# Kernel tuning notes

Hardware: AMD Instinct MI355X
Metric: run time of the kernel (lower is better)

## Reference

```python
import jax, jax.numpy as jnp
import numpy as np

N = 100_000
E = 3_200_000
NCLASS = 64
TOPK = 16
NHID = 128
DEGREE = 6


def setup_inputs() -> dict:
    key = jax.random.key(0)
    ks = jax.random.split(key, 8)
    x = jax.random.normal(ks[0], (N, NCLASS), dtype=jnp.float32)
    edge_row = jax.random.randint(ks[1], (E,), 0, N, dtype=jnp.int64)
    edge_col = jax.random.randint(ks[2], (E,), 0, N, dtype=jnp.int64)
    edge_val = jax.random.uniform(ks[3], (E,), dtype=jnp.float32) / 32.0  # ~row-normalized
    # torch.nn.Linear init: U(-1/sqrt(fan_in), 1/sqrt(fan_in))
    lim1 = 1.0 / np.sqrt(TOPK)
    lim2 = 1.0 / np.sqrt(NHID)
    W1 = jax.random.uniform(ks[4], (NHID, TOPK), jnp.float32, -lim1, lim1)
    b1 = jnp.zeros((NHID,), jnp.float32)
    W2 = jax.random.uniform(ks[5], (DEGREE, NHID), jnp.float32, -lim2, lim2)
    b2 = jnp.zeros((DEGREE,), jnp.float32)
    return {"x": x, "edge_row": edge_row, "edge_col": edge_col,
            "edge_val": edge_val, "W1": W1, "b1": b1, "W2": W2, "b2": b2}


def _spmm(edge_row, edge_col, edge_val, h):
    # (adj @ h)[i] = sum_{(i,j) in E} val_ij * h[j]
    return jax.ops.segment_sum(edge_val[:, None] * h[edge_col], edge_row,
                               num_segments=N)


def reference(x, edge_row, edge_col, edge_val, W1, b1, W2, b2):
    # gating: softmax over classes -> top-k probs -> small MLP -> hop weights
    p = jax.nn.softmax(x, axis=1)
    tk, _ = jax.lax.top_k(p, TOPK)                       # [N, TOPK]
    h = jax.nn.leaky_relu(tk @ W1.T + b1, 0.1)           # [N, NHID]
    weight = jax.nn.softmax(h @ W2.T + b2, axis=1)       # [N, DEGREE]
    # dropout is identity in eval mode
    out = weight[:, 0:1] * x
    cur = x
    for i in range(DEGREE - 1):
        cur = _spmm(edge_row, edge_col, edge_val, cur)
        out = out + weight[:, i + 1:i + 2] * cur
    return jax.nn.log_softmax(out, axis=1)
```

## Files before the change

kernel.cpp:

```cpp
#include <hip/hip_runtime.h>
#include <math.h>

#define N_NODES 100000
#define N_EDGES 3200000
#define NCLASS  64
#define TOPK    16
#define NHID    128
#define DEG     6

#define NBUCK   391
#define BUCKCAP 9216

__device__ __forceinline__ float bf2f(unsigned short u) {
    return __uint_as_float(((unsigned)u) << 16);
}
__device__ __forceinline__ unsigned short f2bf(float f) {
    unsigned u = __float_as_uint(f);
    u = (u + 0x7FFFu + ((u >> 16) & 1u)) >> 16;
    return (unsigned short)u;
}

__device__ __forceinline__ float wave_max(float v) {
    #pragma unroll
    for (int off = 1; off < 64; off <<= 1) v = fmaxf(v, __shfl_xor(v, off));
    return v;
}
__device__ __forceinline__ float wave_sum(float v) {
    #pragma unroll
    for (int off = 1; off < 64; off <<= 1) v += __shfl_xor(v, off);
    return v;
}

__global__ void phase1_bucket(const int* __restrict__ erow, const int* __restrict__ ecol,
                              const float* __restrict__ eval, int* __restrict__ fill,
                              int2* __restrict__ staging) {
    int i = blockIdx.x * 256 + threadIdx.x;
    if (i < N_EDGES) {
        int   r = __builtin_nontemporal_load(&erow[i]);
        int   c = __builtin_nontemporal_load(&ecol[i]);
        float w = __builtin_nontemporal_load(&eval[i]);
        int b = r >> 8;
        int pos = atomicAdd(&fill[b * 16], 1);
        if (pos < BUCKCAP) {
            int2 e;
            e.x = (c << 8) | (r & 255);
            e.y = __float_as_int(w);
            staging[(size_t)b * BUCKCAP + pos] = e;
        }
    }
}

__global__ void bucket_scan(const int* __restrict__ fill, int* __restrict__ bucket_base,
                            int* __restrict__ row_ptr) {
    __shared__ int sdat[512];
    int tid = threadIdx.x;
    int c = 0;
    if (tid < NBUCK) c = min(fill[tid * 16], BUCKCAP);
    sdat[tid] = c;
    __syncthreads();
    for (int off = 1; off < 512; off <<= 1) {
        int t = (tid >= off) ? sdat[tid - off] : 0;
        __syncthreads();
        sdat[tid] += t;
        __syncthreads();
    }
    if (tid < NBUCK) bucket_base[tid] = sdat[tid] - c;
    if (tid == 0) row_ptr[N_NODES] = sdat[511];
}

__global__ __launch_bounds__(256) void phase2_build(
        const int2* __restrict__ staging, const int* __restrict__ fill,
        const int* __restrict__ bucket_base, int* __restrict__ row_ptr,
        int2* __restrict__ edges_s) {
    __shared__ int lhist[256];
    __shared__ int lscan[256];
    __shared__ int lfill[256];
    int b = blockIdx.x, tid = threadIdx.x;
    int c = min(fill[b * 16], BUCKCAP);
    const int2* seg = staging + (size_t)b * BUCKCAP;
    lhist[tid] = 0;
    __syncthreads();
    for (int j = tid; j < c; j += 256) atomicAdd(&lhist[seg[j].x & 255], 1);
    __syncthreads();
    int v = lhist[tid];
    lscan[tid] = v;
    __syncthreads();
    for (int off = 1; off < 256; off <<= 1) {
        int t = (tid >= off) ? lscan[tid - off] : 0;
        __syncthreads();
        lscan[tid] += t;
        __syncthreads();
    }
    int excl = bucket_base[b] + (lscan[tid] - v);
    int grow = b * 256 + tid;
    if (grow < N_NODES) row_ptr[grow] = excl;
    lfill[tid] = excl;
    __syncthreads();
    for (int j = tid; j < c; j += 256) {
        int2 e = seg[j];
        int rl = e.x & 255;
        int pos = atomicAdd(&lfill[rl], 1);
        edges_s[pos] = make_int2((int)(((unsigned)e.x) >> 8), e.y);
    }
}

#define GNODES 32
__global__ __launch_bounds__(256) void gating_kernel(
        const float* __restrict__ x,  const float* __restrict__ W1,
        const float* __restrict__ b1, const float* __restrict__ W2,
        const float* __restrict__ b2, float* __restrict__ weight,
        float* __restrict__ out_acc, unsigned short* __restrict__ xbf) {
    __shared__ float sW1t[TOPK * NHID];
    __shared__ float sb1[NHID];
    __shared__ float sW2[DEG * NHID];
    __shared__ float sb2[DEG];
    int tid = threadIdx.x;
    for (int idx = tid; idx < NHID * TOPK; idx += 256) {
        int k = idx / NHID, j = idx - k * NHID;
        sW1t[idx] = W1[j * TOPK + k];
    }
    for (int i = tid; i < NHID; i += 256) sb1[i] = b1[i];
    for (int i = tid; i < DEG * NHID; i += 256) sW2[i] = W2[i];
    if (tid < DEG) sb2[tid] = b2[tid];
    __syncthreads();

    int wave = tid >> 6;
    int lane = tid & 63;

    for (int it = 0; it < GNODES / 4; it++) {
        int node = blockIdx.x * GNODES + it * 4 + wave;
        if (node >= N_NODES) continue;

        float xv = x[node * NCLASS + lane];
        xbf[node * NCLASS + lane] = f2bf(xv);

        float v = xv;
        #pragma unroll
        for (int k = 2; k <= 64; k <<= 1) {
            #pragma unroll
            for (int j = k >> 1; j > 0; j >>= 1) {
                float o = __shfl_xor(v, j);
                bool keep_small = (((lane & j) == 0) == ((lane & k) == 0));
                v = keep_small ? fminf(v, o) : fmaxf(v, o);
            }
        }
        float m = __shfl(v, 63);
        float e = __expf(v - m);
        float s = wave_sum(e);
        float inv_s = 1.0f / s;

        float h0 = sb1[lane], h1 = sb1[lane + 64];
        #pragma unroll
        for (int k = 0; k < TOPK; k++) {
            float sv = __shfl(v, 63 - k);
            float tk = __expf(sv - m) * inv_s;
            h0 += tk * sW1t[k * NHID + lane];
            h1 += tk * sW1t[k * NHID + lane + 64];
        }
        h0 = (h0 > 0.f) ? h0 : 0.1f * h0;
        h1 = (h1 > 0.f) ? h1 : 0.1f * h1;

        float w[DEG];
        float wm = -1e30f;
        #pragma unroll
        for (int d = 0; d < DEG; d++) {
            float part = h0 * sW2[d * NHID + lane] + h1 * sW2[d * NHID + lane + 64];
            w[d] = wave_sum(part) + sb2[d];
            wm = fmaxf(wm, w[d]);
        }
        float wsum = 0.f;
        #pragma unroll
        for (int d = 0; d < DEG; d++) { w[d] = __expf(w[d] - wm); wsum += w[d]; }
        float inv = 1.0f / wsum;

        if (lane < DEG) weight[node * DEG + lane] = w[lane] * inv;
        out_acc[node * NCLASS + lane] = w[0] * inv * xv;
    }
}

__device__ __forceinline__ void gather8(const unsigned short* __restrict__ src,
                                        const long long* __restrict__ edq,
                                        int e, int lane, float& acc) {
    long long q[8];
    #pragma unroll
    for (int k = 0; k < 8; k++) q[k] = __builtin_nontemporal_load(&edq[e + k]);
    float vk[8], fk[8];
    #pragma unroll
    for (int k = 0; k < 8; k++) {
        int col = __builtin_amdgcn_readfirstlane((int)(unsigned)q[k]);
        vk[k] = __int_as_float(__builtin_amdgcn_readfirstlane((int)(q[k] >> 32)));
        fk[k] = bf2f(src[col * NCLASS + lane]);
    }
    #pragma unroll
    for (int k = 0; k < 8; k++) acc += vk[k] * fk[k];
}

__device__ __forceinline__ void gather4(const unsigned short* __restrict__ src,
                                        const long long* __restrict__ edq,
                                        int e, int lane, float& acc) {
    long long q[4];
    #pragma unroll
    for (int k = 0; k < 4; k++) q[k] = __builtin_nontemporal_load(&edq[e + k]);
    float vk[4], fk[4];
    #pragma unroll
    for (int k = 0; k < 4; k++) {
        int col = __builtin_amdgcn_readfirstlane((int)(unsigned)q[k]);
        vk[k] = __int_as_float(__builtin_amdgcn_readfirstlane((int)(q[k] >> 32)));
        fk[k] = bf2f(src[col * NCLASS + lane]);
    }
    #pragma unroll
    for (int k = 0; k < 4; k++) acc += vk[k] * fk[k];
}

__device__ __forceinline__ float drain_row(const unsigned short* __restrict__ src,
                                           const long long* __restrict__ edq,
                                           int e, int end, int lane, float acc) {
    for (; e + 4 <= end; e += 4) gather4(src, edq, e, lane, acc);
    for (; e < end; e++) {
        long long q0 = __builtin_nontemporal_load(&edq[e]);
        int   c0 = __builtin_amdgcn_readfirstlane((int)(unsigned)q0);
        float v0 = __int_as_float(__builtin_amdgcn_readfirstlane((int)(q0 >> 32)));
        acc += v0 * bf2f(src[c0 * NCLASS + lane]);
    }
    return acc;
}

__global__ __launch_bounds__(256) void spmm_kernel(
        const unsigned short* __restrict__ src, unsigned short* __restrict__ dst,
        const int* __restrict__ row_ptr, const int2* __restrict__ edges_s,
        const float* __restrict__ weight,
        float* __restrict__ out_acc, float* __restrict__ final_out,
        int hop, int mode) {
    int wave = threadIdx.x >> 6;
    int lane = threadIdx.x & 63;
    int wid = blockIdx.x * 4 + wave;
    int rA = wid * 2;
    if (rA >= N_NODES) return;
    int rB = rA + 1;

    int sA   = __builtin_amdgcn_readfirstlane(row_ptr[rA]);
    int endA = __builtin_amdgcn_readfirstlane(row_ptr[rA + 1]);
    int endB = __builtin_amdgcn_readfirstlane(row_ptr[rA + 2]);

    const long long* edq = (const long long*)edges_s;
    float accA = 0.f, accB = 0.f;
    int eA = sA, eB = endA;
    while (eA + 8 <= endA && eB + 8 <= endB) {
        gather8(src, edq, eA, lane, accA);
        gather8(src, edq, eB, lane, accB);
        eA += 8; eB += 8;
    }
    accA = drain_row(src, edq, eA, endA, lane, accA);
    accB = drain_row(src, edq, eB, endB, lane, accB);

    float wA = weight[rA * DEG + hop];
    float wB = weight[rB * DEG + hop];
    if (mode == 0) {
        dst[rA * NCLASS + lane] = f2bf(accA);
        dst[rB * NCLASS + lane] = f2bf(accB);
    } else if (mode == 1) {
        dst[rA * NCLASS + lane] = f2bf(accA);
        dst[rB * NCLASS + lane] = f2bf(accB);
        float pA = bf2f(src[rA * NCLASS + lane]);
        float pB = bf2f(src[rB * NCLASS + lane]);
        float wpA = weight[rA * DEG + hop - 1];
        float wpB = weight[rB * DEG + hop - 1];
        out_acc[rA * NCLASS + lane] += wpA * pA + wA * accA;
        out_acc[rB * NCLASS + lane] += wpB * pB + wB * accB;
    } else {
        float vA = out_acc[rA * NCLASS + lane] + wA * accA;
        float mA = wave_max(vA);
        float eA2 = __expf(vA - mA);
        float sA2 = wave_sum(eA2);
        final_out[rA * NCLASS + lane] = vA - mA - __logf(sA2);

        float vB = out_acc[rB * NCLASS + lane] + wB * accB;
        float mB = wave_max(vB);
        float eB2 = __expf(vB - mB);
        float sB2 = wave_sum(eB2);
        final_out[rB * NCLASS + lane] = vB - mB - __logf(sB2);
    }
}

extern "C" void kernel_launch(void* const* d_in, const int* in_sizes, int n_in,
                              void* d_out, int out_size, void* d_ws, size_t ws_size,
                              hipStream_t stream) {
    const float* x    = (const float*)d_in[0];
    const int*   erow = (const int*)  d_in[1];
    const int*   ecol = (const int*)  d_in[2];
    const float* eval = (const float*)d_in[3];
    const float* W1   = (const float*)d_in[4];
    const float* b1   = (const float*)d_in[5];
    const float* W2   = (const float*)d_in[6];
    const float* b2   = (const float*)d_in[7];
    float* out = (float*)d_out;

    char* ws = (char*)d_ws;
    size_t off = 0;
    auto alloc = [&](size_t bytes) -> void* {
        void* p = ws + off;
        off = (off + bytes + 255) & ~(size_t)255;
        return p;
    };
    char* regionA = (char*)alloc((size_t)N_NODES * NCLASS * 2 * 3);
    int2* staging = (int2*)regionA;
    unsigned short* xbf  = (unsigned short*)regionA;
    unsigned short* cur0 = (unsigned short*)(regionA + (size_t)N_NODES * NCLASS * 2);
    unsigned short* cur1 = (unsigned short*)(regionA + (size_t)N_NODES * NCLASS * 4);

    int2*  edges_s     = (int2*)alloc((size_t)N_EDGES * 8);
    int*   row_ptr     = (int*) alloc((size_t)(N_NODES + 1) * 4);
    int*   fill        = (int*) alloc((size_t)NBUCK * 16 * 4);
    int*   bucket_base = (int*) alloc((size_t)NBUCK * 4);
    float* weight      = (float*)alloc((size_t)N_NODES * DEG * 4);

    const int EB = (N_EDGES + 255) / 256;
    const int WB = ((N_NODES / 2) + 3) / 4;
    const int GB = (N_NODES + GNODES - 1) / GNODES;

    hipMemsetAsync(fill, 0, (size_t)NBUCK * 16 * 4, stream);
    phase1_bucket<<<EB, 256, 0, stream>>>(erow, ecol, eval, fill, staging);
    bucket_scan<<<1, 512, 0, stream>>>(fill, bucket_base, row_ptr);
    phase2_build<<<NBUCK, 256, 0, stream>>>(staging, fill, bucket_base, row_ptr, edges_s);

    gating_kernel<<<GB, 256, 0, stream>>>(x, W1, b1, W2, b2, weight, out, xbf);

    spmm_kernel<<<WB, 256, 0, stream>>>(xbf,  cur0, row_ptr, edges_s, weight, out, out, 1, 0);
    spmm_kernel<<<WB, 256, 0, stream>>>(cur0, cur1, row_ptr, edges_s, weight, out, out, 2, 1);
    spmm_kernel<<<WB, 256, 0, stream>>>(cur1, cur0, row_ptr, edges_s, weight, out, out, 3, 0);
    spmm_kernel<<<WB, 256, 0, stream>>>(cur0, cur1, row_ptr, edges_s, weight, out, out, 4, 1);
    spmm_kernel<<<WB, 256, 0, stream>>>(cur1, cur0, row_ptr, edges_s, weight, out, out, 5, 2);
}
```

Baseline: 722.1 us.

## Fuse edge bucketing with gating, split bucket atomics, fold accumulation into final hop

Merges the edge-bucketing pass and the gating MLP into one launch by partitioning the grid. Bucket fill counters are split into 8 sub-segments so fewer edges contend on each atomic. The separate scan kernel is dropped, and each build block instead computes its own base by summing the counts of earlier buckets. Hop 4 no longer does its out_acc read-modify-write; the final hop reads the two previous hop outputs and applies their weights, which saves a full pass over the fp32 accumulator. The costs are redundant prefix work in every build block and larger staging capacity limits, since edges beyond a sub-segment's capacity are silently dropped.

```diff
diff --git a/kernel.cpp b/kernel.cpp
--- a/kernel.cpp
+++ b/kernel.cpp
@@ -9,7 +9,12 @@
 #define DEG     6
 
 #define NBUCK   391
-#define BUCKCAP 9216
+#define NSEG    8
+#define SEGCAP  1408
+
+#define EB ((N_EDGES + 255) / 256)
+#define GNODES 32
+#define GB ((N_NODES + GNODES - 1) / GNODES)
 
 __device__ __forceinline__ float bf2f(unsigned short u) {
     return __uint_as_float(((unsigned)u) << 16);
@@ -31,81 +36,10 @@
     return v;
 }
 
-__global__ void phase1_bucket(const int* __restrict__ erow, const int* __restrict__ ecol,
-                              const float* __restrict__ eval, int* __restrict__ fill,
-                              int2* __restrict__ staging) {
-    int i = blockIdx.x * 256 + threadIdx.x;
-    if (i < N_EDGES) {
-        int   r = __builtin_nontemporal_load(&erow[i]);
-        int   c = __builtin_nontemporal_load(&ecol[i]);
-        float w = __builtin_nontemporal_load(&eval[i]);
-        int b = r >> 8;
-        int pos = atomicAdd(&fill[b * 16], 1);
-        if (pos < BUCKCAP) {
-            int2 e;
-            e.x = (c << 8) | (r & 255);
-            e.y = __float_as_int(w);
-            staging[(size_t)b * BUCKCAP + pos] = e;
-        }
-    }
-}
-
-__global__ void bucket_scan(const int* __restrict__ fill, int* __restrict__ bucket_base,
-                            int* __restrict__ row_ptr) {
-    __shared__ int sdat[512];
-    int tid = threadIdx.x;
-    int c = 0;
-    if (tid < NBUCK) c = min(fill[tid * 16], BUCKCAP);
-    sdat[tid] = c;
-    __syncthreads();
-    for (int off = 1; off < 512; off <<= 1) {
-        int t = (tid >= off) ? sdat[tid - off] : 0;
-        __syncthreads();
-        sdat[tid] += t;
-        __syncthreads();
-    }
-    if (tid < NBUCK) bucket_base[tid] = sdat[tid] - c;
-    if (tid == 0) row_ptr[N_NODES] = sdat[511];
-}
-
-__global__ __launch_bounds__(256) void phase2_build(
-        const int2* __restrict__ staging, const int* __restrict__ fill,
-        const int* __restrict__ bucket_base, int* __restrict__ row_ptr,
-        int2* __restrict__ edges_s) {
-    __shared__ int lhist[256];
-    __shared__ int lscan[256];
-    __shared__ int lfill[256];
-    int b = blockIdx.x, tid = threadIdx.x;
-    int c = min(fill[b * 16], BUCKCAP);
-    const int2* seg = staging + (size_t)b * BUCKCAP;
-    lhist[tid] = 0;
-    __syncthreads();
-    for (int j = tid; j < c; j += 256) atomicAdd(&lhist[seg[j].x & 255], 1);
-    __syncthreads();
-    int v = lhist[tid];
-    lscan[tid] = v;
-    __syncthreads();
-    for (int off = 1; off < 256; off <<= 1) {
-        int t = (tid >= off) ? lscan[tid - off] : 0;
-        __syncthreads();
-        lscan[tid] += t;
-        __syncthreads();
-    }
-    int excl = bucket_base[b] + (lscan[tid] - v);
-    int grow = b * 256 + tid;
-    if (grow < N_NODES) row_ptr[grow] = excl;
-    lfill[tid] = excl;
-    __syncthreads();
-    for (int j = tid; j < c; j += 256) {
-        int2 e = seg[j];
-        int rl = e.x & 255;
-        int pos = atomicAdd(&lfill[rl], 1);
-        edges_s[pos] = make_int2((int)(((unsigned)e.x) >> 8), e.y);
-    }
-}
-
-#define GNODES 32
-__global__ __launch_bounds__(256) void gating_kernel(
+__global__ __launch_bounds__(256) void scatter_gating_kernel(
+        const int* __restrict__ erow, const int* __restrict__ ecol,
+        const float* __restrict__ eval, int* __restrict__ fill,
+        int2* __restrict__ staging,
         const float* __restrict__ x,  const float* __restrict__ W1,
         const float* __restrict__ b1, const float* __restrict__ W2,
         const float* __restrict__ b2, float* __restrict__ weight,
@@ -114,6 +48,26 @@
     __shared__ float sb1[NHID];
     __shared__ float sW2[DEG * NHID];
     __shared__ float sb2[DEG];
+
+    if (blockIdx.x < EB) {
+        int i = blockIdx.x * 256 + threadIdx.x;
+        int s = blockIdx.x & 7;
+        if (i < N_EDGES) {
+            int   r = __builtin_nontemporal_load(&erow[i]);
+            int   c = __builtin_nontemporal_load(&ecol[i]);
+            float w = __builtin_nontemporal_load(&eval[i]);
+            int b = r >> 8;
+            int pos = atomicAdd(&fill[(s * NBUCK + b) * 16], 1);
+            if (pos < SEGCAP) {
+                int2 e;
+                e.x = (c << 8) | (r & 255);
+                e.y = __float_as_int(w);
+                staging[((size_t)b * NSEG + s) * SEGCAP + pos] = e;
+            }
+        }
+        return;
+    }
+
     int tid = threadIdx.x;
     for (int idx = tid; idx < NHID * TOPK; idx += 256) {
         int k = idx / NHID, j = idx - k * NHID;
@@ -126,9 +80,10 @@
 
     int wave = tid >> 6;
     int lane = tid & 63;
+    int gb = blockIdx.x - EB;
 
     for (int it = 0; it < GNODES / 4; it++) {
-        int node = blockIdx.x * GNODES + it * 4 + wave;
+        int node = gb * GNODES + it * 4 + wave;
         if (node >= N_NODES) continue;
 
         float xv = x[node * NCLASS + lane];
@@ -175,6 +130,67 @@
 
         if (lane < DEG) weight[node * DEG + lane] = w[lane] * inv;
         out_acc[node * NCLASS + lane] = w[0] * inv * xv;
+    }
+}
+
+__global__ __launch_bounds__(256) void phase2_build(
+        const int2* __restrict__ staging, const int* __restrict__ fill,
+        int* __restrict__ row_ptr, int2* __restrict__ edges_s) {
+    __shared__ int lred[256];
+    __shared__ int lhist[256];
+    __shared__ int lscan[256];
+    __shared__ int lfill[256];
+    __shared__ int sseg[NSEG];
+    int b = blockIdx.x, tid = threadIdx.x;
+
+    int part = 0;
+    for (int j = tid; j < b; j += 256) {
+        int t = 0;
+        #pragma unroll
+        for (int s = 0; s < NSEG; s++) t += min(fill[(s * NBUCK + j) * 16], SEGCAP);
+        part += t;
+    }
+    lred[tid] = part;
+    if (tid < NSEG) sseg[tid] = min(fill[(tid * NBUCK + b) * 16], SEGCAP);
+    __syncthreads();
+    for (int off = 128; off > 0; off >>= 1) {
+        if (tid < off) lred[tid] += lred[tid + off];
+        __syncthreads();
+    }
+    int base_b = lred[0];
+
+    lhist[tid] = 0;
+    __syncthreads();
+    for (int s = 0; s < NSEG; s++) {
+        int c = sseg[s];
+        const int2* seg = staging + ((size_t)b * NSEG + s) * SEGCAP;
+        for (int j = tid; j < c; j += 256) atomicAdd(&lhist[seg[j].x & 255], 1);
+    }
+    __syncthreads();
+    int v = lhist[tid];
+    lscan[tid] = v;
+    __syncthreads();
+    for (int off = 1; off < 256; off <<= 1) {
+        int t = (tid >= off) ? lscan[tid - off] : 0;
+        __syncthreads();
+        lscan[tid] += t;
+        __syncthreads();
+    }
+    int excl = base_b + (lscan[tid] - v);
+    int grow = b * 256 + tid;
+    if (grow < N_NODES) row_ptr[grow] = excl;
+    if (b == NBUCK - 1 && tid == 255) row_ptr[N_NODES] = excl + v;
+    lfill[tid] = excl;
+    __syncthreads();
+    for (int s = 0; s < NSEG; s++) {
+        int c = sseg[s];
+        const int2* seg = staging + ((size_t)b * NSEG + s) * SEGCAP;
+        for (int j = tid; j < c; j += 256) {
+            int2 e = seg[j];
+            int rl = e.x & 255;
+            int pos = atomicAdd(&lfill[rl], 1);
+            edges_s[pos] = make_int2((int)(((unsigned)e.x) >> 8), e.y);
+        }
     }
 }
 
@@ -227,6 +243,7 @@
 
 __global__ __launch_bounds__(256) void spmm_kernel(
         const unsigned short* __restrict__ src, unsigned short* __restrict__ dst,
+        const unsigned short* __restrict__ prev2,
         const int* __restrict__ row_ptr, const int2* __restrict__ edges_s,
         const float* __restrict__ weight,
         float* __restrict__ out_acc, float* __restrict__ final_out,
@@ -268,13 +285,21 @@
         out_acc[rA * NCLASS + lane] += wpA * pA + wA * accA;
         out_acc[rB * NCLASS + lane] += wpB * pB + wB * accB;
     } else {
-        float vA = out_acc[rA * NCLASS + lane] + wA * accA;
+        float p1A = bf2f(src[rA * NCLASS + lane]);
+        float p1B = bf2f(src[rB * NCLASS + lane]);
+        float p2A = bf2f(prev2[rA * NCLASS + lane]);
+        float p2B = bf2f(prev2[rB * NCLASS + lane]);
+        float vA = out_acc[rA * NCLASS + lane]
+                 + weight[rA * DEG + hop - 2] * p2A
+                 + weight[rA * DEG + hop - 1] * p1A + wA * accA;
         float mA = wave_max(vA);
         float eA2 = __expf(vA - mA);
         float sA2 = wave_sum(eA2);
         final_out[rA * NCLASS + lane] = vA - mA - __logf(sA2);
 
-        float vB = out_acc[rB * NCLASS + lane] + wB * accB;
+        float vB = out_acc[rB * NCLASS + lane]
+                 + weight[rB * DEG + hop - 2] * p2B
+                 + weight[rB * DEG + hop - 1] * p1B + wB * accB;
         float mB = wave_max(vB);
         float eB2 = __expf(vB - mB);
         float sB2 = wave_sum(eB2);
@@ -302,32 +327,27 @@
         off = (off + bytes + 255) & ~(size_t)255;
         return p;
     };
-    char* regionA = (char*)alloc((size_t)N_NODES * NCLASS * 2 * 3);
-    int2* staging = (int2*)regionA;
-    unsigned short* xbf  = (unsigned short*)regionA;
-    unsigned short* cur0 = (unsigned short*)(regionA + (size_t)N_NODES * NCLASS * 2);
-    unsigned short* cur1 = (unsigned short*)(regionA + (size_t)N_NODES * NCLASS * 4);
-
-    int2*  edges_s     = (int2*)alloc((size_t)N_EDGES * 8);
-    int*   row_ptr     = (int*) alloc((size_t)(N_NODES + 1) * 4);
-    int*   fill        = (int*) alloc((size_t)NBUCK * 16 * 4);
-    int*   bucket_base = (int*) alloc((size_t)NBUCK * 4);
-    float* weight      = (float*)alloc((size_t)N_NODES * DEG * 4);
-
-    const int EB = (N_EDGES + 255) / 256;
+    char* regionS = (char*)alloc((size_t)NBUCK * NSEG * SEGCAP * 8);
+    int2* staging = (int2*)regionS;
+    unsigned short* cur0 = (unsigned short*)regionS;
+    unsigned short* cur1 = (unsigned short*)(regionS + (size_t)N_NODES * NCLASS * 2);
+    unsigned short* xbf  = (unsigned short*)alloc((size_t)N_NODES * NCLASS * 2);
+
+    int2*  edges_s = (int2*)alloc((size_t)N_EDGES * 8);
+    int*   row_ptr = (int*) alloc((size_t)(N_NODES + 1) * 4);
+    int*   fill    = (int*) alloc((size_t)NSEG * NBUCK * 16 * 4);
+    float* weight  = (float*)alloc((size_t)N_NODES * DEG * 4);
+
     const int WB = ((N_NODES / 2) + 3) / 4;
-    const int GB = (N_NODES + GNODES - 1) / GNODES;
-
-    hipMemsetAsync(fill, 0, (size_t)NBUCK * 16 * 4, stream);
-    phase1_bucket<<<EB, 256, 0, stream>>>(erow, ecol, eval, fill, staging);
-    bucket_scan<<<1, 512, 0, stream>>>(fill, bucket_base, row_ptr);
-    phase2_build<<<NBUCK, 256, 0, stream>>>(staging, fill, bucket_base, row_ptr, edges_s);
-
-    gating_kernel<<<GB, 256, 0, stream>>>(x, W1, b1, W2, b2, weight, out, xbf);
-
-    spmm_kernel<<<WB, 256, 0, stream>>>(xbf,  cur0, row_ptr, edges_s, weight, out, out, 1, 0);
-    spmm_kernel<<<WB, 256, 0, stream>>>(cur0, cur1, row_ptr, edges_s, weight, out, out, 2, 1);
-    spmm_kernel<<<WB, 256, 0, stream>>>(cur1, cur0, row_ptr, edges_s, weight, out, out, 3, 0);
-    spmm_kernel<<<WB, 256, 0, stream>>>(cur0, cur1, row_ptr, edges_s, weight, out, out, 4, 1);
-    spmm_kernel<<<WB, 256, 0, stream>>>(cur1, cur0, row_ptr, edges_s, weight, out, out, 5, 2);
-}
+
+    hipMemsetAsync(fill, 0, (size_t)NSEG * NBUCK * 16 * 4, stream);
+    scatter_gating_kernel<<<EB + GB, 256, 0, stream>>>(
+        erow, ecol, eval, fill, staging, x, W1, b1, W2, b2, weight, out, xbf);
+    phase2_build<<<NBUCK, 256, 0, stream>>>(staging, fill, row_ptr, edges_s);
+
+    spmm_kernel<<<WB, 256, 0, stream>>>(xbf,  cur0, cur0, row_ptr, edges_s, weight, out, out, 1, 0);
+    spmm_kernel<<<WB, 256, 0, stream>>>(cur0, cur1, cur0, row_ptr, edges_s, weight, out, out, 2, 1);
+    spmm_kernel<<<WB, 256, 0, stream>>>(cur1, cur0, cur0, row_ptr, edges_s, weight, out, out, 3, 0);
+    spmm_kernel<<<WB, 256, 0, stream>>>(cur0, cur1, cur0, row_ptr, edges_s, weight, out, out, 4, 0);
+    spmm_kernel<<<WB, 256, 0, stream>>>(cur1, cur0, cur0, row_ptr, edges_s, weight, out, out, 5, 3);
+}
```

Result: faster. 682.4 us (-5.5%).
